# Optimization experiments

Hardware: AMD Instinct MI355X
Metric: run time of the kernel (lower is better)

The kernel has to match this reference:

```python
import jax, jax.numpy as jnp
import numpy as np

VOCAB, E, H, OUT = 128, 768, 768, 768
B, T = 128, 512


def setup_inputs() -> dict:
    key = jax.random.key(0)
    ks = jax.random.split(key, 8)
    s_emb = 1.0  # torch nn.Embedding default init is N(0,1)
    s_gru = 1.0 / np.sqrt(H)  # torch GRU init U(-1/sqrt(H), 1/sqrt(H))
    s_fc = 1.0 / np.sqrt(H)
    return {
        "x": jax.random.randint(ks[0], (B, T), 0, VOCAB),
        "emb": jax.random.normal(ks[1], (VOCAB, E), dtype=jnp.float32) * s_emb,
        "W_ih": jax.random.uniform(ks[2], (3 * H, E), jnp.float32, -s_gru, s_gru),
        "W_hh": jax.random.uniform(ks[3], (3 * H, H), jnp.float32, -s_gru, s_gru),
        "b_ih": jax.random.uniform(ks[4], (3 * H,), jnp.float32, -s_gru, s_gru),
        "b_hh": jax.random.uniform(ks[5], (3 * H,), jnp.float32, -s_gru, s_gru),
        "fc_W": jax.random.uniform(ks[6], (OUT, H), jnp.float32, -s_fc, s_fc),
        "fc_b": jax.random.uniform(ks[7], (OUT,), jnp.float32, -s_fc, s_fc),
    }


def _gru_last_hidden(xe, W_ih, W_hh, b_ih, b_hh):
    # xe: [B, T, E]. Precompute all input-side gate pre-activations in one GEMM.
    gx = jnp.einsum("bte,ge->btg", xe, W_ih) + b_ih  # [B, T, 3H]
    gx = jnp.swapaxes(gx, 0, 1)  # [T, B, 3H] for scan
    h0 = jnp.zeros((xe.shape[0], W_hh.shape[1]), xe.dtype)

    def step(h, gx_t):
        gh = h @ W_hh.T + b_hh  # [B, 3H]
        xr, xz, xn = jnp.split(gx_t, 3, axis=-1)
        hr, hz, hn = jnp.split(gh, 3, axis=-1)
        r = jax.nn.sigmoid(xr + hr)
        z = jax.nn.sigmoid(xz + hz)
        n = jnp.tanh(xn + r * hn)
        h_new = (1.0 - z) * n + z * h
        return h_new, None

    h_last, _ = jax.lax.scan(step, h0, gx)
    return h_last  # [B, H]


def reference(x, emb, W_ih, W_hh, b_ih, b_hh, fc_W, fc_b):
    xe = jnp.take(emb, x, axis=0)  # [B, T, E]
    h = _gru_last_hidden(xe, W_ih, W_hh, b_ih, b_hh)
    return h @ fc_W.T + fc_b  # [B, OUT]
```

## Files before the change

kernel.cpp:

```cpp
#include <hip/hip_runtime.h>

#define DI __device__ __forceinline__

constexpr int BB   = 128;
constexpr int TT   = 512;
constexpr int HH   = 768;
constexpr int G3   = 3 * HH;
constexpr int VOC  = 128;

constexpr int NG   = 8;
constexpr int NW   = 48;
constexpr int KC   = 24;
constexpr int FPAD = 16;

constexpr size_t OFF_GE   = 0;
constexpr size_t OFF_WIMG = 1179648;
constexpr size_t OFF_H16  = OFF_WIMG + 3538944;
constexpr size_t OFF_H32  = OFF_H16 + 393216;
constexpr size_t OFF_FLG  = OFF_H32 + 393216;

constexpr int LDS_W_BYTES = 3 * KC * 64 * 16;
constexpr int LDS_BYTES   = LDS_W_BYTES + 1024;

typedef _Float16 f16x8 __attribute__((ext_vector_type(8)));
typedef float    f32x4 __attribute__((ext_vector_type(4)));

DI float sigm(float x) { return __builtin_amdgcn_rcpf(1.0f + __expf(-x)); }
DI float tanh_fast(float x) {
  float e = __expf(-2.0f * fabsf(x));
  float r = (1.0f - e) * __builtin_amdgcn_rcpf(1.0f + e);
  return copysignf(r, x);
}

DI f16x8 load_dc_x4(const void* p) {
  f16x8 r;
  asm volatile("global_load_dwordx4 %0, %1, off sc1"
               : "=v"(r) : "v"(p) : "memory");
  return r;
}
DI void store_dc_x2(void* p, uint2 v) {
  asm volatile("global_store_dwordx2 %0, %1, off sc1"
               :: "v"(p), "v"(v) : "memory");
}
DI int load_flag(const int* p) {
  int r;
  asm volatile("global_load_dword %0, %1, off sc1\n\ts_waitcnt vmcnt(0)"
               : "=v"(r) : "v"(p) : "memory");
  return r;
}
DI void store_flag(int* p, int v) {
  asm volatile("global_store_dword %0, %1, off sc1"
               :: "v"(p), "v"(v) : "memory");
}
DI void wait_vm0() { asm volatile("s_waitcnt vmcnt(0)" ::: "memory"); }
DI void wait_lgkm0() { asm volatile("s_waitcnt lgkmcnt(0)" ::: "memory"); }

__global__ void k_zero(int* flg, int n) {
  int i = blockIdx.x * 256 + threadIdx.x;
  if (i < n) flg[i] = 0;
}

__global__ void k_prep_w(const float* __restrict__ Whh, _Float16* __restrict__ wimg) {
  int tid = blockIdx.x * 256 + threadIdx.x;
  if (tid >= NW * 3 * KC * 64) return;
  int l  = tid & 63;
  int fi = tid >> 6;
  int kc = fi % KC;
  int nt = (fi / KC) % 3;
  int j  = fi / (KC * 3);
  int g  = nt * HH + j * 16 + (l & 15);
  int k0 = kc * 32 + (l >> 4) * 8;
  const float* src = Whh + (size_t)g * HH + k0;
  f16x8 o;
#pragma unroll
  for (int q = 0; q < 8; ++q) o[q] = (_Float16)src[q];
  ((f16x8*)wimg)[tid] = o;
}

__global__ void k_prep_ge(const float* __restrict__ emb, const float* __restrict__ Wih,
                          const float* __restrict__ bih, float* __restrict__ ge) {
  int g  = blockIdx.x * 256 + threadIdx.x;
  int v0 = blockIdx.y * 16;
  float acc[16];
  float b = bih[g];
#pragma unroll
  for (int i = 0; i < 16; ++i) acc[i] = b;
  const float* wrow = Wih + (size_t)g * HH;
  for (int e = 0; e < HH; e += 4) {
    float4 w = *(const float4*)(wrow + e);
#pragma unroll
    for (int i = 0; i < 16; ++i) {
      float4 m = *(const float4*)(emb + (size_t)(v0 + i) * HH + e);
      acc[i] = fmaf(w.x, m.x, acc[i]);
      acc[i] = fmaf(w.y, m.y, acc[i]);
      acc[i] = fmaf(w.z, m.z, acc[i]);
      acc[i] = fmaf(w.w, m.w, acc[i]);
    }
  }
#pragma unroll
  for (int i = 0; i < 16; ++i) ge[(size_t)(v0 + i) * G3 + g] = acc[i];
}

__global__ __launch_bounds__(64, 1) void k_gru(
    const int* __restrict__ x,
    const float* __restrict__ ge,
    const float* __restrict__ bhh,
    const _Float16* __restrict__ wimg,
    _Float16* h16,
    float* __restrict__ h32,
    int* flg)
{
  extern __shared__ char smem[];
  _Float16* st = (_Float16*)(smem + LDS_W_BYTES);

  const int lane = threadIdx.x;
  const int bid  = blockIdx.x;
  const int grp  = bid / NW;
  const int j    = bid % NW;
  const int bm   = grp * 16;
  const int u0   = j * 16;
  int* gflg = flg + grp * NW * FPAD;

  {
    const uint4* src = (const uint4*)(wimg + (size_t)j * (3 * KC * 64 * 8));
    uint4* dst = (uint4*)smem;
#pragma unroll 8
    for (int r = 0; r < 72; ++r) dst[lane + 64 * r] = src[lane + 64 * r];
  }

  const int c16 = lane & 15;
  const int kr  = lane >> 4;

  const float bh_r = bhh[0 * HH + u0 + c16];
  const float bh_z = bhh[1 * HH + u0 + c16];
  const float bh_n = bhh[2 * HH + u0 + c16];

  float hprev[4] = {0.f, 0.f, 0.f, 0.f};

  _Float16* hb0 = h16;
  _Float16* hb1 = h16 + (size_t)BB * HH;
  const f16x8* bfr = (const f16x8*)smem;

  const int fidx = (lane < NW) ? lane : (lane - NW);
  const int* fpoll = gflg + fidx * FPAD;

  float ger[4], gez[4], gen[4];
#pragma unroll
  for (int q = 0; q < 4; ++q) {
    int xv = x[(size_t)(bm + kr * 4 + q) * TT + 0];
    const float* gp = ge + (size_t)xv * G3 + u0 + c16;
    ger[q] = gp[0 * HH];
    gez[q] = gp[1 * HH];
    gen[q] = gp[2 * HH];
  }

  int budget = 1 << 20;

  for (int t = 0; t < TT; ++t) {
    int xvn[4];
    if (t < TT - 1) {
#pragma unroll
      for (int q = 0; q < 4; ++q)
        xvn[q] = x[(size_t)(bm + kr * 4 + q) * TT + (t + 1)];
    }

    f32x4 acc0 = {bh_r, bh_r, bh_r, bh_r};
    f32x4 acc1 = {bh_z, bh_z, bh_z, bh_z};
    f32x4 acc2 = {bh_n, bh_n, bh_n, bh_n};

    if (t > 0) {
      for (;;) {
        int f = load_flag(fpoll);
        if (__all(f >= t)) break;
        if (--budget < 0) break;
      }
      asm volatile("" ::: "memory");

      const _Float16* hb = (t & 1) ? hb1 : hb0;
      const char* ab = (const char*)(hb + (size_t)(bm + c16) * HH) + kr * 16;
      f16x8 a[KC];
#pragma unroll
      for (int kc = 0; kc < KC; ++kc) a[kc] = load_dc_x4(ab + kc * 64);
      wait_vm0();
      __builtin_amdgcn_sched_barrier(0);

#pragma unroll
      for (int kc = 0; kc < KC; ++kc) {
        acc0 = __builtin_amdgcn_mfma_f32_16x16x32_f16(a[kc], bfr[(0 * KC + kc) * 64 + lane], acc0, 0, 0, 0);
        acc1 = __builtin_amdgcn_mfma_f32_16x16x32_f16(a[kc], bfr[(1 * KC + kc) * 64 + lane], acc1, 0, 0, 0);
        acc2 = __builtin_amdgcn_mfma_f32_16x16x32_f16(a[kc], bfr[(2 * KC + kc) * 64 + lane], acc2, 0, 0, 0);
      }
    }

    float hv[4];
#pragma unroll
    for (int q = 0; q < 4; ++q) {
      float r = sigm(acc0[q] + ger[q]);
      float z = sigm(acc1[q] + gez[q]);
      float n = tanh_fast(gen[q] + r * acc2[q]);
      float h = n + z * (hprev[q] - n);
      hprev[q] = h;
      hv[q] = h;
    }

    if (t == TT - 1) {
#pragma unroll
      for (int q = 0; q < 4; ++q)
        h32[(size_t)(bm + kr * 4 + q) * HH + u0 + c16] = hv[q];
    } else {
#pragma unroll
      for (int q = 0; q < 4; ++q)
        st[(kr * 4 + q) * 20 + c16] = (_Float16)hv[q];

#pragma unroll
      for (int q = 0; q < 4; ++q) {
        const float* gp = ge + (size_t)xvn[q] * G3 + u0 + c16;
        ger[q] = gp[0 * HH];
        gez[q] = gp[1 * HH];
        gen[q] = gp[2 * HH];
      }

      wait_lgkm0();
      __builtin_amdgcn_sched_barrier(0);
      int rr = lane >> 2;
      int qq = lane & 3;
      uint2 v = *(const uint2*)&st[rr * 20 + qq * 4];
      _Float16* hn = (t & 1) ? hb0 : hb1;
      store_dc_x2((char*)(hn + (size_t)(bm + rr) * HH + u0 + qq * 4), v);

      wait_vm0();
      if (lane == 0) store_flag(gflg + j * FPAD, t + 1);
    }
  }
}

__global__ void k_fc(const float* __restrict__ h32, const float* __restrict__ fcW,
                     const float* __restrict__ fcb, float* __restrict__ out) {
  int o  = blockIdx.x * 256 + threadIdx.x;
  int b0 = blockIdx.y * 16;
  float acc[16];
  float bi = fcb[o];
#pragma unroll
  for (int i = 0; i < 16; ++i) acc[i] = bi;
  const float* wrow = fcW + (size_t)o * HH;
  for (int e = 0; e < HH; e += 4) {
    float4 w = *(const float4*)(wrow + e);
#pragma unroll
    for (int i = 0; i < 16; ++i) {
      float4 m = *(const float4*)(h32 + (size_t)(b0 + i) * HH + e);
      acc[i] = fmaf(w.x, m.x, acc[i]);
      acc[i] = fmaf(w.y, m.y, acc[i]);
      acc[i] = fmaf(w.z, m.z, acc[i]);
      acc[i] = fmaf(w.w, m.w, acc[i]);
    }
  }
#pragma unroll
  for (int i = 0; i < 16; ++i) out[(size_t)(b0 + i) * HH + o] = acc[i];
}

extern "C" void kernel_launch(void* const* d_in, const int* in_sizes, int n_in,
                              void* d_out, int out_size, void* d_ws, size_t ws_size,
                              hipStream_t stream) {
  const int*   x   = (const int*)d_in[0];
  const float* emb = (const float*)d_in[1];
  const float* Wih = (const float*)d_in[2];
  const float* Whh = (const float*)d_in[3];
  const float* bih = (const float*)d_in[4];
  const float* bhh = (const float*)d_in[5];
  const float* fcW = (const float*)d_in[6];
  const float* fcb = (const float*)d_in[7];
  float* out = (float*)d_out;

  char* ws = (char*)d_ws;
  float*     ge   = (float*)(ws + OFF_GE);
  _Float16*  wimg = (_Float16*)(ws + OFF_WIMG);
  _Float16*  h16  = (_Float16*)(ws + OFF_H16);
  float*     h32  = (float*)(ws + OFF_H32);
  int*       flg  = (int*)(ws + OFF_FLG);

  k_zero<<<24, 256, 0, stream>>>(flg, NG * NW * FPAD);
  k_prep_w<<<864, 256, 0, stream>>>(Whh, wimg);
  k_prep_ge<<<dim3(9, 8), 256, 0, stream>>>(emb, Wih, bih, ge);

  hipFuncSetAttribute(reinterpret_cast<const void*>(k_gru),
                      hipFuncAttributeMaxDynamicSharedMemorySize, LDS_BYTES);
  k_gru<<<NG * NW, 64, LDS_BYTES, stream>>>(x, ge, bhh, wimg, h16, h32, flg);

  k_fc<<<dim3(3, 8), 256, 0, stream>>>(h32, fcW, fcb, out);
}
```

Measured before the change: 2.314 ms.

## Split GRU recurrent K-reduction across two waves and pack flags for vector polling

Each GRU block now runs two waves. Each wave computes half of the K chunks of the recurrent h·W_hh MFMA, and wave 1 hands its partial sums to wave 0 through LDS with a block barrier each step. Flags are packed contiguously (64 per group, padding set to INT_MAX), so each lane polls four flags with a single dwordx4 load instead of one padded flag. The aim is to halve the per-step MFMA and h-load latency on the serial critical path. In exchange it adds an LDS exchange and __syncthreads per timestep, and packing flags into shared cache lines may raise contention when producers write them.

```diff
diff --git a/kernel.cpp b/kernel.cpp
--- a/kernel.cpp
+++ b/kernel.cpp
@@ -11,7 +11,7 @@
 constexpr int NG   = 8;
 constexpr int NW   = 48;
 constexpr int KC   = 24;
-constexpr int FPAD = 16;
+constexpr int KCW  = 12;
 
 constexpr size_t OFF_GE   = 0;
 constexpr size_t OFF_WIMG = 1179648;
@@ -20,10 +20,13 @@
 constexpr size_t OFF_FLG  = OFF_H32 + 393216;
 
 constexpr int LDS_W_BYTES = 3 * KC * 64 * 16;
-constexpr int LDS_BYTES   = LDS_W_BYTES + 1024;
+constexpr int LDS_P_OFF   = LDS_W_BYTES;
+constexpr int LDS_S_OFF   = LDS_P_OFF + 6144;
+constexpr int LDS_BYTES   = LDS_S_OFF + 1024;
 
 typedef _Float16 f16x8 __attribute__((ext_vector_type(8)));
 typedef float    f32x4 __attribute__((ext_vector_type(4)));
+typedef unsigned int u32x4 __attribute__((ext_vector_type(4)));
 
 DI float sigm(float x) { return __builtin_amdgcn_rcpf(1.0f + __expf(-x)); }
 DI float tanh_fast(float x) {
@@ -42,9 +45,9 @@
   asm volatile("global_store_dwordx2 %0, %1, off sc1"
                :: "v"(p), "v"(v) : "memory");
 }
-DI int load_flag(const int* p) {
-  int r;
-  asm volatile("global_load_dword %0, %1, off sc1\n\ts_waitcnt vmcnt(0)"
+DI u32x4 load_flags4(const int* p) {
+  u32x4 r;
+  asm volatile("global_load_dwordx4 %0, %1, off sc1\n\ts_waitcnt vmcnt(0)"
                : "=v"(r) : "v"(p) : "memory");
   return r;
 }
@@ -57,7 +60,7 @@
 
 __global__ void k_zero(int* flg, int n) {
   int i = blockIdx.x * 256 + threadIdx.x;
-  if (i < n) flg[i] = 0;
+  if (i < n) flg[i] = ((i & 63) < NW) ? 0 : 0x7fffffff;
 }
 
 __global__ void k_prep_w(const float* __restrict__ Whh, _Float16* __restrict__ wimg) {
@@ -101,7 +104,7 @@
   for (int i = 0; i < 16; ++i) ge[(size_t)(v0 + i) * G3 + g] = acc[i];
 }
 
-__global__ __launch_bounds__(64, 1) void k_gru(
+__global__ __launch_bounds__(128, 1) void k_gru(
     const int* __restrict__ x,
     const float* __restrict__ ge,
     const float* __restrict__ bhh,
@@ -111,29 +114,33 @@
     int* flg)
 {
   extern __shared__ char smem[];
-  _Float16* st = (_Float16*)(smem + LDS_W_BYTES);
-
-  const int lane = threadIdx.x;
+  float*    part = (float*)(smem + LDS_P_OFF);
+  _Float16* st   = (_Float16*)(smem + LDS_S_OFF);
+
+  const int tid  = threadIdx.x;
+  const int lane = tid & 63;
+  const int wid  = tid >> 6;
   const int bid  = blockIdx.x;
   const int grp  = bid / NW;
   const int j    = bid % NW;
   const int bm   = grp * 16;
   const int u0   = j * 16;
-  int* gflg = flg + grp * NW * FPAD;
+  int* gflg = flg + grp * 64;
 
   {
     const uint4* src = (const uint4*)(wimg + (size_t)j * (3 * KC * 64 * 8));
     uint4* dst = (uint4*)smem;
-#pragma unroll 8
-    for (int r = 0; r < 72; ++r) dst[lane + 64 * r] = src[lane + 64 * r];
+#pragma unroll 6
+    for (int r = 0; r < 36; ++r) dst[tid + 128 * r] = src[tid + 128 * r];
   }
 
   const int c16 = lane & 15;
   const int kr  = lane >> 4;
-
-  const float bh_r = bhh[0 * HH + u0 + c16];
-  const float bh_z = bhh[1 * HH + u0 + c16];
-  const float bh_n = bhh[2 * HH + u0 + c16];
+  const int kc0 = wid * KCW;
+
+  const float bh_r = (wid == 0) ? bhh[0 * HH + u0 + c16] : 0.0f;
+  const float bh_z = (wid == 0) ? bhh[1 * HH + u0 + c16] : 0.0f;
+  const float bh_n = (wid == 0) ? bhh[2 * HH + u0 + c16] : 0.0f;
 
   float hprev[4] = {0.f, 0.f, 0.f, 0.f};
 
@@ -141,8 +148,7 @@
   _Float16* hb1 = h16 + (size_t)BB * HH;
   const f16x8* bfr = (const f16x8*)smem;
 
-  const int fidx = (lane < NW) ? lane : (lane - NW);
-  const int* fpoll = gflg + fidx * FPAD;
+  const int* fpoll = gflg + (lane & 15) * 4;
 
   float ger[4], gez[4], gen[4];
 #pragma unroll
@@ -154,82 +160,93 @@
     gen[q] = gp[2 * HH];
   }
 
+  __syncthreads();
   int budget = 1 << 20;
 
   for (int t = 0; t < TT; ++t) {
-    int xvn[4];
-    if (t < TT - 1) {
-#pragma unroll
-      for (int q = 0; q < 4; ++q)
-        xvn[q] = x[(size_t)(bm + kr * 4 + q) * TT + (t + 1)];
-    }
-
     f32x4 acc0 = {bh_r, bh_r, bh_r, bh_r};
     f32x4 acc1 = {bh_z, bh_z, bh_z, bh_z};
     f32x4 acc2 = {bh_n, bh_n, bh_n, bh_n};
 
     if (t > 0) {
       for (;;) {
-        int f = load_flag(fpoll);
-        if (__all(f >= t)) break;
+        u32x4 f = load_flags4(fpoll);
+        int m0 = min((int)f.x, (int)f.y);
+        int m1 = min((int)f.z, (int)f.w);
+        if (__all(min(m0, m1) >= t)) break;
         if (--budget < 0) break;
       }
       asm volatile("" ::: "memory");
 
       const _Float16* hb = (t & 1) ? hb1 : hb0;
-      const char* ab = (const char*)(hb + (size_t)(bm + c16) * HH) + kr * 16;
-      f16x8 a[KC];
-#pragma unroll
-      for (int kc = 0; kc < KC; ++kc) a[kc] = load_dc_x4(ab + kc * 64);
+      const char* ab = (const char*)(hb + (size_t)(bm + c16) * HH) + kr * 16 + kc0 * 64;
+      f16x8 a[KCW];
+#pragma unroll
+      for (int kc = 0; kc < KCW; ++kc) a[kc] = load_dc_x4(ab + kc * 64);
       wait_vm0();
       __builtin_amdgcn_sched_barrier(0);
 
 #pragma unroll
-      for (int kc = 0; kc < KC; ++kc) {
-        acc0 = __builtin_amdgcn_mfma_f32_16x16x32_f16(a[kc], bfr[(0 * KC + kc) * 64 + lane], acc0, 0, 0, 0);
-        acc1 = __builtin_amdgcn_mfma_f32_16x16x32_f16(a[kc], bfr[(1 * KC + kc) * 64 + lane], acc1, 0, 0, 0);
-        acc2 = __builtin_amdgcn_mfma_f32_16x16x32_f16(a[kc], bfr[(2 * KC + kc) * 64 + lane], acc2, 0, 0, 0);
+      for (int kc = 0; kc < KCW; ++kc) {
+        acc0 = __builtin_amdgcn_mfma_f32_16x16x32_f16(a[kc], bfr[(0 * KC + kc0 + kc) * 64 + lane], acc0, 0, 0, 0);
+        acc1 = __builtin_amdgcn_mfma_f32_16x16x32_f16(a[kc], bfr[(1 * KC + kc0 + kc) * 64 + lane], acc1, 0, 0, 0);
+        acc2 = __builtin_amdgcn_mfma_f32_16x16x32_f16(a[kc], bfr[(2 * KC + kc0 + kc) * 64 + lane], acc2, 0, 0, 0);
       }
     }
 
-    float hv[4];
-#pragma unroll
-    for (int q = 0; q < 4; ++q) {
-      float r = sigm(acc0[q] + ger[q]);
-      float z = sigm(acc1[q] + gez[q]);
-      float n = tanh_fast(gen[q] + r * acc2[q]);
-      float h = n + z * (hprev[q] - n);
-      hprev[q] = h;
-      hv[q] = h;
-    }
-
-    if (t == TT - 1) {
-#pragma unroll
-      for (int q = 0; q < 4; ++q)
-        h32[(size_t)(bm + kr * 4 + q) * HH + u0 + c16] = hv[q];
-    } else {
-#pragma unroll
-      for (int q = 0; q < 4; ++q)
-        st[(kr * 4 + q) * 20 + c16] = (_Float16)hv[q];
-
+    if (wid == 1) {
+      float* pp = part + (t & 1) * 768 + lane * 12;
+      *(f32x4*)(pp + 0) = acc0;
+      *(f32x4*)(pp + 4) = acc1;
+      *(f32x4*)(pp + 8) = acc2;
+    }
+    __syncthreads();
+
+    if (wid == 0) {
+      const float* pp = part + (t & 1) * 768 + lane * 12;
+      acc0 += *(const f32x4*)(pp + 0);
+      acc1 += *(const f32x4*)(pp + 4);
+      acc2 += *(const f32x4*)(pp + 8);
+
+      float hv[4];
 #pragma unroll
       for (int q = 0; q < 4; ++q) {
-        const float* gp = ge + (size_t)xvn[q] * G3 + u0 + c16;
-        ger[q] = gp[0 * HH];
-        gez[q] = gp[1 * HH];
-        gen[q] = gp[2 * HH];
+        float r = sigm(acc0[q] + ger[q]);
+        float z = sigm(acc1[q] + gez[q]);
+        float n = tanh_fast(gen[q] + r * acc2[q]);
+        float h = n + z * (hprev[q] - n);
+        hprev[q] = h;
+        hv[q] = h;
       }
 
-      wait_lgkm0();
-      __builtin_amdgcn_sched_barrier(0);
-      int rr = lane >> 2;
-      int qq = lane & 3;
-      uint2 v = *(const uint2*)&st[rr * 20 + qq * 4];
-      _Float16* hn = (t & 1) ? hb0 : hb1;
-      store_dc_x2((char*)(hn + (size_t)(bm + rr) * HH + u0 + qq * 4), v);
-
-      wait_vm0();
-      if (lane == 0) store_flag(gflg + j * FPAD, t + 1);
+      if (t == TT - 1) {
+#pragma unroll
+        for (int q = 0; q < 4; ++q)
+          h32[(size_t)(bm + kr * 4 + q) * HH + u0 + c16] = hv[q];
+      } else {
+#pragma unroll
+        for (int q = 0; q < 4; ++q)
+          st[(kr * 4 + q) * 20 + c16] = (_Float16)hv[q];
+        wait_lgkm0();
+        __builtin_amdgcn_sched_barrier(0);
+        int rr = lane >> 2;
+        int qq = lane & 3;
+        uint2 v = *(const uint2*)&st[rr * 20 + qq * 4];
+        _Float16* hn = (t & 1) ? hb0 : hb1;
+        store_dc_x2((char*)(hn + (size_t)(bm + rr) * HH + u0 + qq * 4), v);
+
+        wait_vm0();
+        if (lane == 0) store_flag(gflg + j, t + 1);
+
+#pragma unroll
+        for (int q = 0; q < 4; ++q) {
+          int xv = x[(size_t)(bm + kr * 4 + q) * TT + (t + 1)];
+          const float* gp = ge + (size_t)xv * G3 + u0 + c16;
+          ger[q] = gp[0 * HH];
+          gez[q] = gp[1 * HH];
+          gen[q] = gp[2 * HH];
+        }
+      }
     }
   }
 }
@@ -278,13 +295,13 @@
   float*     h32  = (float*)(ws + OFF_H32);
   int*       flg  = (int*)(ws + OFF_FLG);
 
-  k_zero<<<24, 256, 0, stream>>>(flg, NG * NW * FPAD);
+  k_zero<<<2, 256, 0, stream>>>(flg, NG * 64);
   k_prep_w<<<864, 256, 0, stream>>>(Whh, wimg);
   k_prep_ge<<<dim3(9, 8), 256, 0, stream>>>(emb, Wih, bih, ge);
 
   hipFuncSetAttribute(reinterpret_cast<const void*>(k_gru),
                       hipFuncAttributeMaxDynamicSharedMemorySize, LDS_BYTES);
-  k_gru<<<NG * NW, 64, LDS_BYTES, stream>>>(x, ge, bhh, wimg, h16, h32, flg);
+  k_gru<<<NG * NW, 128, LDS_BYTES, stream>>>(x, ge, bhh, wimg, h16, h32, flg);
 
   k_fc<<<dim3(3, 8), 256, 0, stream>>>(h32, fcW, fcb, out);
 }
```

Measured after the change: 3.849 ms. 66.3% more time.

## Add per-group coordinator blocks that aggregate step flags into epoch words

Applied to the files above, without the earlier changes.

Adds NG coordinator workgroups to the persistent GRU kernel. Each one polls the 48 per-block step flags of its batch group and then publishes a per-block epoch value. Worker blocks now poll a single epoch word instead of each wave polling all 48 flags, which cuts polling traffic on the flag lines. The cost is an extra hop of latency on every timestep's barrier, plus 8 more resident blocks that also need the large LDS allocation and must be co-resident with the workers to avoid deadlock.

```diff
diff --git a/kernel.cpp b/kernel.cpp
--- a/kernel.cpp
+++ b/kernel.cpp
@@ -18,6 +18,7 @@
 constexpr size_t OFF_H16  = OFF_WIMG + 3538944;
 constexpr size_t OFF_H32  = OFF_H16 + 393216;
 constexpr size_t OFF_FLG  = OFF_H32 + 393216;
+constexpr size_t OFF_EPO  = OFF_FLG + 24576;
 
 constexpr int LDS_W_BYTES = 3 * KC * 64 * 16;
 constexpr int LDS_BYTES   = LDS_W_BYTES + 1024;
@@ -55,9 +56,9 @@
 DI void wait_vm0() { asm volatile("s_waitcnt vmcnt(0)" ::: "memory"); }
 DI void wait_lgkm0() { asm volatile("s_waitcnt lgkmcnt(0)" ::: "memory"); }
 
-__global__ void k_zero(int* flg, int n) {
+__global__ void k_zero(int* p, int n) {
   int i = blockIdx.x * 256 + threadIdx.x;
-  if (i < n) flg[i] = 0;
+  if (i < n) p[i] = 0;
 }
 
 __global__ void k_prep_w(const float* __restrict__ Whh, _Float16* __restrict__ wimg) {
@@ -108,18 +109,39 @@
     const _Float16* __restrict__ wimg,
     _Float16* h16,
     float* __restrict__ h32,
-    int* flg)
+    int* flg,
+    int* epo)
 {
   extern __shared__ char smem[];
   _Float16* st = (_Float16*)(smem + LDS_W_BYTES);
 
   const int lane = threadIdx.x;
   const int bid  = blockIdx.x;
-  const int grp  = bid / NW;
-  const int j    = bid % NW;
+
+  if (bid < NG) {
+    const int g = bid;
+    const int fidx = (lane < NW) ? lane : (lane - NW);
+    const int* fp = flg + (g * NW + fidx) * FPAD;
+    int* ep = epo + g * NW * FPAD;
+    long budget = 1L << 22;
+    for (int e = 1; e <= TT - 1; ++e) {
+      for (;;) {
+        int f = load_flag(fp);
+        if (__all(f >= e)) break;
+        if (--budget < 0) break;
+      }
+      if (lane < NW) store_flag(ep + lane * FPAD, e);
+    }
+    return;
+  }
+
+  const int w    = bid - NG;
+  const int grp  = w / NW;
+  const int j    = w % NW;
   const int bm   = grp * 16;
   const int u0   = j * 16;
   int* gflg = flg + grp * NW * FPAD;
+  const int* myep = epo + (grp * NW + j) * FPAD;
 
   {
     const uint4* src = (const uint4*)(wimg + (size_t)j * (3 * KC * 64 * 8));
@@ -140,9 +162,6 @@
   _Float16* hb0 = h16;
   _Float16* hb1 = h16 + (size_t)BB * HH;
   const f16x8* bfr = (const f16x8*)smem;
-
-  const int fidx = (lane < NW) ? lane : (lane - NW);
-  const int* fpoll = gflg + fidx * FPAD;
 
   float ger[4], gez[4], gen[4];
 #pragma unroll
@@ -170,8 +189,8 @@
 
     if (t > 0) {
       for (;;) {
-        int f = load_flag(fpoll);
-        if (__all(f >= t)) break;
+        int e = load_flag(myep);
+        if (e >= t) break;
         if (--budget < 0) break;
       }
       asm volatile("" ::: "memory");
@@ -277,14 +296,15 @@
   _Float16*  h16  = (_Float16*)(ws + OFF_H16);
   float*     h32  = (float*)(ws + OFF_H32);
   int*       flg  = (int*)(ws + OFF_FLG);
-
-  k_zero<<<24, 256, 0, stream>>>(flg, NG * NW * FPAD);
+  int*       epo  = (int*)(ws + OFF_EPO);
+
+  k_zero<<<48, 256, 0, stream>>>(flg, 2 * NG * NW * FPAD);
   k_prep_w<<<864, 256, 0, stream>>>(Whh, wimg);
   k_prep_ge<<<dim3(9, 8), 256, 0, stream>>>(emb, Wih, bih, ge);
 
   hipFuncSetAttribute(reinterpret_cast<const void*>(k_gru),
                       hipFuncAttributeMaxDynamicSharedMemorySize, LDS_BYTES);
-  k_gru<<<NG * NW, 64, LDS_BYTES, stream>>>(x, ge, bhh, wimg, h16, h32, flg);
+  k_gru<<<NG * NW + NG, 64, LDS_BYTES, stream>>>(x, ge, bhh, wimg, h16, h32, flg, epo);
 
   k_fc<<<dim3(3, 8), 256, 0, stream>>>(h32, fcW, fcb, out);
 }
```

Result: slower. 2.371 ms (+2.5%).

## Replace flag-based step sync with poisoned ring buffer polling on hidden state

Applied to the files above, without the earlier changes.

Removes the per-step flag store and flag polling. Hidden-state exchange now goes through an 8-slot ring per batch group that is pre-filled with f16 infinity/NaN sentinels. Consumers repeatedly load the hidden-state chunks until no loaded value matches the sentinel exponent pattern, and producers re-poison a slot a few steps ahead. This takes the flag round-trip and the store-then-wait-then-flag serialization off the recurrent critical path. The cost is repeated data reloads while waiting, and correctness now depends on the sentinel never appearing in real values and on per-load ordering, since only lanes x and z of each 16-byte load are checked.

```diff
diff --git a/kernel.cpp b/kernel.cpp
--- a/kernel.cpp
+++ b/kernel.cpp
@@ -11,19 +11,23 @@
 constexpr int NG   = 8;
 constexpr int NW   = 48;
 constexpr int KC   = 24;
-constexpr int FPAD = 16;
+constexpr int CRING = 8;
+
+constexpr int ROWB = HH * 2;
+constexpr int SLOT = 16 * ROWB;
+constexpr size_t GR_RING = (size_t)CRING * SLOT;
 
 constexpr size_t OFF_GE   = 0;
 constexpr size_t OFF_WIMG = 1179648;
-constexpr size_t OFF_H16  = OFF_WIMG + 3538944;
-constexpr size_t OFF_H32  = OFF_H16 + 393216;
-constexpr size_t OFF_FLG  = OFF_H32 + 393216;
+constexpr size_t OFF_RING = OFF_WIMG + 3538944;
+constexpr size_t OFF_H32  = OFF_RING + NG * GR_RING;
 
 constexpr int LDS_W_BYTES = 3 * KC * 64 * 16;
 constexpr int LDS_BYTES   = LDS_W_BYTES + 1024;
 
 typedef _Float16 f16x8 __attribute__((ext_vector_type(8)));
 typedef float    f32x4 __attribute__((ext_vector_type(4)));
+typedef unsigned int u32x4 __attribute__((ext_vector_type(4)));
 
 DI float sigm(float x) { return __builtin_amdgcn_rcpf(1.0f + __expf(-x)); }
 DI float tanh_fast(float x) {
@@ -42,22 +46,13 @@
   asm volatile("global_store_dwordx2 %0, %1, off sc1"
                :: "v"(p), "v"(v) : "memory");
 }
-DI int load_flag(const int* p) {
-  int r;
-  asm volatile("global_load_dword %0, %1, off sc1\n\ts_waitcnt vmcnt(0)"
-               : "=v"(r) : "v"(p) : "memory");
-  return r;
-}
-DI void store_flag(int* p, int v) {
-  asm volatile("global_store_dword %0, %1, off sc1"
-               :: "v"(p), "v"(v) : "memory");
-}
 DI void wait_vm0() { asm volatile("s_waitcnt vmcnt(0)" ::: "memory"); }
 DI void wait_lgkm0() { asm volatile("s_waitcnt lgkmcnt(0)" ::: "memory"); }
 
-__global__ void k_zero(int* flg, int n) {
+__global__ void k_poison(u32x4* ring, int n16) {
   int i = blockIdx.x * 256 + threadIdx.x;
-  if (i < n) flg[i] = 0;
+  u32x4 p = {0x7C007C00u, 0x7C007C00u, 0x7C007C00u, 0x7C007C00u};
+  if (i < n16) ring[i] = p;
 }
 
 __global__ void k_prep_w(const float* __restrict__ Whh, _Float16* __restrict__ wimg) {
@@ -106,9 +101,8 @@
     const float* __restrict__ ge,
     const float* __restrict__ bhh,
     const _Float16* __restrict__ wimg,
-    _Float16* h16,
-    float* __restrict__ h32,
-    int* flg)
+    char* ring,
+    float* __restrict__ h32)
 {
   extern __shared__ char smem[];
   _Float16* st = (_Float16*)(smem + LDS_W_BYTES);
@@ -119,7 +113,7 @@
   const int j    = bid % NW;
   const int bm   = grp * 16;
   const int u0   = j * 16;
-  int* gflg = flg + grp * NW * FPAD;
+  char* gring = ring + (size_t)grp * GR_RING;
 
   {
     const uint4* src = (const uint4*)(wimg + (size_t)j * (3 * KC * 64 * 8));
@@ -136,13 +130,12 @@
   const float bh_n = bhh[2 * HH + u0 + c16];
 
   float hprev[4] = {0.f, 0.f, 0.f, 0.f};
-
-  _Float16* hb0 = h16;
-  _Float16* hb1 = h16 + (size_t)BB * HH;
   const f16x8* bfr = (const f16x8*)smem;
 
-  const int fidx = (lane < NW) ? lane : (lane - NW);
-  const int* fpoll = gflg + fidx * FPAD;
+  const int rr = lane >> 2;
+  const int qq = lane & 3;
+  const size_t pub_off = (size_t)rr * ROWB + (u0 + qq * 4) * 2;
+  const size_t con_off = (size_t)c16 * ROWB + kr * 16;
 
   float ger[4], gez[4], gen[4];
 #pragma unroll
@@ -169,19 +162,26 @@
     f32x4 acc2 = {bh_n, bh_n, bh_n, bh_n};
 
     if (t > 0) {
+      const char* ab = gring + (size_t)(t & 7) * SLOT + con_off;
+      f16x8 a[KC];
+      unsigned vm = 0;
       for (;;) {
-        int f = load_flag(fpoll);
-        if (__all(f >= t)) break;
+#pragma unroll
+        for (int kc = 0; kc < KC; ++kc)
+          if (!((vm >> kc) & 1u)) a[kc] = load_dc_x4(ab + kc * 64);
+        wait_vm0();
+        __builtin_amdgcn_sched_barrier(0);
+#pragma unroll
+        for (int kc = 0; kc < KC; ++kc)
+          if (!((vm >> kc) & 1u)) {
+            u32x4 u = *(const u32x4*)&a[kc];
+            unsigned ok = ((u.x & 0x7C00u) != 0x7C00u) &
+                          ((u.z & 0x7C00u) != 0x7C00u);
+            vm |= ok << kc;
+          }
+        if (__all(vm == 0xFFFFFFu)) break;
         if (--budget < 0) break;
       }
-      asm volatile("" ::: "memory");
-
-      const _Float16* hb = (t & 1) ? hb1 : hb0;
-      const char* ab = (const char*)(hb + (size_t)(bm + c16) * HH) + kr * 16;
-      f16x8 a[KC];
-#pragma unroll
-      for (int kc = 0; kc < KC; ++kc) a[kc] = load_dc_x4(ab + kc * 64);
-      wait_vm0();
       __builtin_amdgcn_sched_barrier(0);
 
 #pragma unroll
@@ -211,6 +211,13 @@
 #pragma unroll
       for (int q = 0; q < 4; ++q)
         st[(kr * 4 + q) * 20 + c16] = (_Float16)hv[q];
+      wait_lgkm0();
+      __builtin_amdgcn_sched_barrier(0);
+      uint2 v = *(const uint2*)&st[rr * 20 + qq * 4];
+
+      store_dc_x2(gring + (size_t)((t + 1) & 7) * SLOT + pub_off, v);
+      uint2 pz; pz.x = 0x7C007C00u; pz.y = 0x7C007C00u;
+      store_dc_x2(gring + (size_t)((t + 6) & 7) * SLOT + pub_off, pz);
 
 #pragma unroll
       for (int q = 0; q < 4; ++q) {
@@ -219,17 +226,6 @@
         gez[q] = gp[1 * HH];
         gen[q] = gp[2 * HH];
       }
-
-      wait_lgkm0();
-      __builtin_amdgcn_sched_barrier(0);
-      int rr = lane >> 2;
-      int qq = lane & 3;
-      uint2 v = *(const uint2*)&st[rr * 20 + qq * 4];
-      _Float16* hn = (t & 1) ? hb0 : hb1;
-      store_dc_x2((char*)(hn + (size_t)(bm + rr) * HH + u0 + qq * 4), v);
-
-      wait_vm0();
-      if (lane == 0) store_flag(gflg + j * FPAD, t + 1);
     }
   }
 }
@@ -274,17 +270,16 @@
   char* ws = (char*)d_ws;
   float*     ge   = (float*)(ws + OFF_GE);
   _Float16*  wimg = (_Float16*)(ws + OFF_WIMG);
-  _Float16*  h16  = (_Float16*)(ws + OFF_H16);
+  char*      ring = ws + OFF_RING;
   float*     h32  = (float*)(ws + OFF_H32);
-  int*       flg  = (int*)(ws + OFF_FLG);
-
-  k_zero<<<24, 256, 0, stream>>>(flg, NG * NW * FPAD);
+
+  k_poison<<<384, 256, 0, stream>>>((u32x4*)ring, 98304);
   k_prep_w<<<864, 256, 0, stream>>>(Whh, wimg);
   k_prep_ge<<<dim3(9, 8), 256, 0, stream>>>(emb, Wih, bih, ge);
 
   hipFuncSetAttribute(reinterpret_cast<const void*>(k_gru),
                       hipFuncAttributeMaxDynamicSharedMemorySize, LDS_BYTES);
-  k_gru<<<NG * NW, 64, LDS_BYTES, stream>>>(x, ge, bhh, wimg, h16, h32, flg);
+  k_gru<<<NG * NW, 64, LDS_BYTES, stream>>>(x, ge, bhh, wimg, ring, h32);
 
   k_fc<<<dim3(3, 8), 256, 0, stream>>>(h32, fcW, fcb, out);
 }
```

Measured after the change: 2.968 ms. 1.28x slower.
